# Performance work log

Hardware: AMD Instinct MI355X
Metric: run time of the kernel (lower is better)

Reference implementation:

```python
import jax, jax.numpy as jnp
import numpy as np

TEMP1, TEMP2, TEMP3 = 4.0, 5.0, 10.0  # forward() default temps
EPS = 1e-8


def setup_inputs() -> dict:
    key = jax.random.key(0)
    k1, k2 = jax.random.split(key)
    B, L, D = 64, 64, 512
    return {
        "ecg_embs": jax.random.normal(k1, (B, L, D), dtype=jnp.float32),
        "sent_embs": jax.random.normal(k2, (B, L, D), dtype=jnp.float32),
    }


def reference(ecg_embs, sent_embs):
    # Fully-batched version of the original per-sample Python loop.
    # i indexes the sentence (query) sample, j the ecg (context) sample.
    B, L, D = ecg_embs.shape
    # scores[i,j,s,q] = <ecg[j,s,:], sent[i,q,:]>  == contextT @ query in torch
    scores = jnp.einsum('jsd,iqd->ijsq', ecg_embs, sent_embs)
    # 1st softmax over query axis q
    attn = jax.nn.softmax(scores, axis=-1)
    # transpose to (i,j,q,s), temperature-scale, 2nd softmax over source axis s
    attn = jax.nn.softmax(TEMP1 * jnp.swapaxes(attn, -1, -2), axis=-1)  # (i,j,q,s)
    # weightedContext[i,j,q,:] = sum_s attn[i,j,q,s] * ecg[j,s,:]
    wctx = jnp.einsum('ijqs,jsd->ijqd', attn, ecg_embs)
    sent = sent_embs[:, None]  # (i,1,q,d) broadcast over j
    w12 = jnp.sum(sent * wctx, axis=-1)
    w1 = jnp.linalg.norm(sent, axis=-1)
    w2 = jnp.linalg.norm(wctx, axis=-1)
    cos = w12 / jnp.maximum(w1 * w2, EPS)  # (i,j,q)
    # row_sim.mul_(temp2).exp_().sum(dim=1).log() ; similarities[j,i] (cat along dim=1)
    sim = TEMP3 * jnp.log(jnp.sum(jnp.exp(TEMP2 * cos), axis=-1)).T  # (j,i)
    labels = jnp.arange(B)
    logp0 = jax.nn.log_softmax(sim, axis=-1)
    logp1 = jax.nn.log_softmax(sim.T, axis=-1)
    loss0 = -jnp.mean(logp0[labels, labels])
    loss1 = -jnp.mean(logp1[labels, labels])
    # att_maps: list of attn[i] from iteration i == diagonal (i==j) attention,
    # each shaped (1, queryL, ih=1, iw=sourceL); stacked -> (B, 1, L, 1, L)
    att_maps = attn[labels, labels][:, None, :, None, :]
    return (loss0 + loss1) / 2.0, att_maps
```

## Files before the change

kernel.cpp:

```cpp
#include <hip/hip_runtime.h>
#include <math.h>

typedef __attribute__((ext_vector_type(8))) short short8;
typedef __attribute__((ext_vector_type(4))) float f32x4;
typedef unsigned int uint;
typedef unsigned short ushort;

#define T1 4.0f
#define T2 5.0f
#define T3 10.0f
#define EPSF 1e-8f
#define SST 68

__device__ inline ushort f2bf(float x) {
    union { float f; uint u; } a; a.f = x;
    uint r = a.u + 0x7FFFu + ((a.u >> 16) & 1u);
    return (ushort)(r >> 16);
}
__device__ inline float bf2f(ushort h) {
    union { uint u; float f; } a; a.u = ((uint)h) << 16;
    return a.f;
}

#define GLDS(gsrc, ldst) \
    __builtin_amdgcn_global_load_lds( \
        (const __attribute__((address_space(1))) uint*)(gsrc), \
        (__attribute__((address_space(3))) uint*)(ldst), 16, 0, 0)

__global__ __launch_bounds__(256) void prep_kernel(
        const float* __restrict__ ecg, const float* __restrict__ sent,
        char* __restrict__ EH, char* __restrict__ EL,
        char* __restrict__ SH, char* __restrict__ SL, float* __restrict__ w1) {
    __shared__ float partial[256];
    const int bid = blockIdx.x;
    const int tensor = bid >> 6, idx = bid & 63;
    const float* src = (tensor ? sent : ecg) + (size_t)idx * 32768;
    char* dh = (tensor ? SH : EH) + (size_t)idx * 65536;
    char* dl = (tensor ? SL : EL) + (size_t)idx * 65536;
    const int tid = threadIdx.x;
    const int r = tid & 63;
    float s2 = 0.f;
    #pragma unroll
    for (int it = 0; it < 4; it++) {
        int kc = it * 4 + (tid >> 6);
        const float* p = src + r * 512 + kc * 32;
        char* oh = dh + kc * 4096 + r * 64;
        char* ol = dl + kc * 4096 + r * 64;
        #pragma unroll
        for (int c = 0; c < 4; c++) {
            float4 v0 = *(const float4*)(p + c * 8);
            float4 v1 = *(const float4*)(p + c * 8 + 4);
            float x[8] = {v0.x, v0.y, v0.z, v0.w, v1.x, v1.y, v1.z, v1.w};
            uint hw[4], lw[4];
            #pragma unroll
            for (int e = 0; e < 4; e++) {
                float a0 = x[2 * e], a1 = x[2 * e + 1];
                ushort h0 = f2bf(a0), h1 = f2bf(a1);
                hw[e] = (uint)h0 | ((uint)h1 << 16);
                ushort l0 = f2bf(a0 - bf2f(h0)), l1 = f2bf(a1 - bf2f(h1));
                lw[e] = (uint)l0 | ((uint)l1 << 16);
                s2 += a0 * a0 + a1 * a1;
            }
            int phys = (c + (r >> 1)) & 3;
            uint4 H; H.x = hw[0]; H.y = hw[1]; H.z = hw[2]; H.w = hw[3];
            *(uint4*)(oh + phys * 16) = H;
            uint4 L; L.x = lw[0]; L.y = lw[1]; L.z = lw[2]; L.w = lw[3];
            *(uint4*)(ol + phys * 16) = L;
        }
    }
    partial[tid] = s2;
    __syncthreads();
    if (tensor == 1 && tid < 64) {
        float t = partial[tid] + partial[tid + 64] + partial[tid + 128] + partial[tid + 192];
        w1[idx * 64 + tid] = sqrtf(t);
    }
}

__global__ __launch_bounds__(256) void gprep_kernel(
        const char* __restrict__ EH, const char* __restrict__ EL, char* __restrict__ Gp) {
    __shared__ __align__(16) char lds[8192];
    const int j = blockIdx.x;
    const int tid = threadIdx.x;
    const int wv = tid >> 6, lane = tid & 63;
    const int wq = wv >> 1, wn = wv & 1;
    const int quad = lane >> 4, ln = lane & 15;
    const char* srcH = EH + (size_t)j * 65536 + wv * 1024 + lane * 16;
    const char* srcL = EL + (size_t)j * 65536 + wv * 1024 + lane * 16;

    int ao[2], bo[2];
    #pragma unroll
    for (int mi = 0; mi < 2; mi++) {
        int R = 32 * wq + 16 * mi + ln;
        ao[mi] = R * 64 + ((quad + (R >> 1)) & 3) * 16;
    }
    #pragma unroll
    for (int ni = 0; ni < 2; ni++) {
        int R = 32 * wn + 16 * ni + ln;
        bo[ni] = R * 64 + ((quad + (R >> 1)) & 3) * 16;
    }

    f32x4 acc[2][2];
    #pragma unroll
    for (int a = 0; a < 2; a++)
        #pragma unroll
        for (int b = 0; b < 2; b++) acc[a][b] = (f32x4){0.f, 0.f, 0.f, 0.f};

    for (int kc = 0; kc < 16; kc++) {
        GLDS(srcH + (size_t)kc * 4096, lds + wv * 1024);
        GLDS(srcL + (size_t)kc * 4096, lds + 4096 + wv * 1024);
        __syncthreads();
        short8 ah[2], al[2], bh[2], bl[2];
        #pragma unroll
        for (int mi = 0; mi < 2; mi++) {
            ah[mi] = *(const short8*)(lds + ao[mi]);
            al[mi] = *(const short8*)(lds + 4096 + ao[mi]);
        }
        #pragma unroll
        for (int ni = 0; ni < 2; ni++) {
            bh[ni] = *(const short8*)(lds + bo[ni]);
            bl[ni] = *(const short8*)(lds + 4096 + bo[ni]);
        }
        #pragma unroll
        for (int mi = 0; mi < 2; mi++)
            #pragma unroll
            for (int ni = 0; ni < 2; ni++) {
                acc[mi][ni] = __builtin_amdgcn_mfma_f32_16x16x32_bf16(ah[mi], bh[ni], acc[mi][ni], 0, 0, 0);
                acc[mi][ni] = __builtin_amdgcn_mfma_f32_16x16x32_bf16(ah[mi], bl[ni], acc[mi][ni], 0, 0, 0);
                acc[mi][ni] = __builtin_amdgcn_mfma_f32_16x16x32_bf16(al[mi], bh[ni], acc[mi][ni], 0, 0, 0);
            }
        __syncthreads();
    }
    #pragma unroll
    for (int mi = 0; mi < 2; mi++)
        #pragma unroll
        for (int ni = 0; ni < 2; ni++)
            #pragma unroll
            for (int r = 0; r < 4; r++) {
                int t = 32 * wq + 16 * mi + quad * 4 + r;
                int u = 32 * wn + 16 * ni + ln;
                float g = acc[mi][ni][r];
                ushort h = f2bf(g);
                ushort l = f2bf(g - bf2f(h));
                char* base = Gp + (size_t)j * 16384 + t * 128 + (((u >> 3) + t) & 7) * 16 + (u & 7) * 2;
                *(ushort*)base = h;
                *(ushort*)(base + 8192) = l;
            }
}

__global__ __launch_bounds__(256, 4) void pair_kernel(
        const char* __restrict__ EH, const char* __restrict__ EL,
        const char* __restrict__ SH, const char* __restrict__ SL,
        const char* __restrict__ Gp, const float* __restrict__ w1g,
        float* __restrict__ simval, float* __restrict__ out) {

    __shared__ __align__(16) char lds[33792];
    __shared__ __align__(16) float mz[64];
    __shared__ float w12all[256], w2all[256];

    const int tid = threadIdx.x;
    const int bn = blockIdx.x;
    const int xcd = bn & 7, slot = bn >> 3;
    const int T = xcd * 8 + (slot >> 4);
    const int wp = slot & 15;
    const int bi = (T >> 3) * 4 + (wp >> 2);
    const int bj = (T & 7) * 4 + (wp & 3);
    const int i0 = bi * 2, j0 = bj * 2;

    const int wv = tid >> 6, lane = tid & 63;
    const int wq = wv >> 1, wn = wv & 1;
    const int quad = lane >> 4, ln = lane & 15;

    int aoff[4], boff[4];
    #pragma unroll
    for (int mi = 0; mi < 4; mi++) {
        int R = 64 * (mi >> 1) + 32 * wq + 16 * (mi & 1) + ln;
        aoff[mi] = R * 64 + ((quad + (R >> 1)) & 3) * 16;
    }
    #pragma unroll
    for (int ni = 0; ni < 4; ni++) {
        int R = 64 * (ni >> 1) + 32 * wn + 16 * (ni & 1) + ln;
        boff[ni] = 16384 + R * 64 + ((quad + (R >> 1)) & 3) * 16;
    }

    const char* gA; const char* gB; int ldoff;
    if (wv == 0)      { gA = EH + (size_t)j0 * 65536;       gB = EH + (size_t)(j0 + 1) * 65536; ldoff = 0; }
    else if (wv == 1) { gA = EL + (size_t)j0 * 65536;       gB = EL + (size_t)(j0 + 1) * 65536; ldoff = 8192; }
    else if (wv == 2) { gA = SH + (size_t)i0 * 65536;       gB = SH + (size_t)(i0 + 1) * 65536; ldoff = 16384; }
    else              { gA = SL + (size_t)i0 * 65536;       gB = SL + (size_t)(i0 + 1) * 65536; ldoff = 24576; }
    gA += lane * 16; gB += lane * 16;

    f32x4 acc[4][4];
    #pragma unroll
    for (int a = 0; a < 4; a++)
        #pragma unroll
        for (int b = 0; b < 4; b++) acc[a][b] = (f32x4){0.f, 0.f, 0.f, 0.f};

    for (int kc = 0; kc < 16; kc++) {
        #pragma unroll
        for (int n = 0; n < 4; n++) GLDS(gA + n * 1024, lds + ldoff + n * 1024);
        #pragma unroll
        for (int n = 0; n < 4; n++) GLDS(gB + n * 1024, lds + ldoff + 4096 + n * 1024);
        gA += 4096; gB += 4096;
        __syncthreads();
        short8 bh[4], bl[4];
        #pragma unroll
        for (int ni = 0; ni < 4; ni++) {
            bh[ni] = *(const short8*)(lds + boff[ni]);
            bl[ni] = *(const short8*)(lds + boff[ni] + 8192);
        }
        #pragma unroll
        for (int mi = 0; mi < 4; mi++) {
            short8 ah = *(const short8*)(lds + aoff[mi]);
            short8 al = *(const short8*)(lds + aoff[mi] + 8192);
            #pragma unroll
            for (int ni = 0; ni < 4; ni++) {
                acc[mi][ni] = __builtin_amdgcn_mfma_f32_16x16x32_bf16(ah, bh[ni], acc[mi][ni], 0, 0, 0);
                acc[mi][ni] = __builtin_amdgcn_mfma_f32_16x16x32_bf16(ah, bl[ni], acc[mi][ni], 0, 0, 0);
                acc[mi][ni] = __builtin_amdgcn_mfma_f32_16x16x32_bf16(al, bh[ni], acc[mi][ni], 0, 0, 0);
            }
        }
        __syncthreads();
    }

    float* SsT = (float*)lds;
    float* yT  = (float*)lds;
    char*  Pb  = lds + 17408;

    #pragma unroll
    for (int pr = 0; pr < 4; pr++) {
        const int a = pr >> 1, b = pr & 1;
        const int i = i0 + b, j = j0 + a;

        #pragma unroll
        for (int dm = 0; dm < 2; dm++)
            #pragma unroll
            for (int dn = 0; dn < 2; dn++) {
                int s0 = 32 * wq + 16 * dm + quad * 4;
                int q  = 32 * wn + 16 * dn + ln;
                *(f32x4*)(SsT + q * SST + s0) = acc[2 * a + dm][2 * b + dn];
            }
        __syncthreads();

        {
            const int s = tid >> 2, c = tid & 3;
            float vv[16]; float m = -1e30f;
            #pragma unroll
            for (int t = 0; t < 16; t++) { vv[t] = SsT[(16 * c + t) * SST + s]; m = fmaxf(m, vv[t]); }
            m = fmaxf(m, __shfl_xor(m, 1));
            m = fmaxf(m, __shfl_xor(m, 2));
            float sum = 0.f;
            #pragma unroll
            for (int t = 0; t < 16; t++) sum += __expf(vv[t] - m);
            sum += __shfl_xor(sum, 1);
            sum += __shfl_xor(sum, 2);
            if (c == 0) mz[s] = m + __logf(sum);
        }
        __syncthreads();

        {
            const int q = tid >> 2, c = tid & 3;
            float sc[16], at[16];
            #pragma unroll
            for (int r4 = 0; r4 < 4; r4++)
                *(f32x4*)(sc + 4 * r4) = *(const f32x4*)(SsT + q * SST + 16 * c + 4 * r4);
            float mzv[16];
            #pragma unroll
            for (int r4 = 0; r4 < 4; r4++)
                *(f32x4*)(mzv + 4 * r4) = *(const f32x4*)(mz + 16 * c + 4 * r4);
            float m2 = -1e30f;
            #pragma unroll
            for (int t = 0; t < 16; t++) {
                at[t] = __expf(sc[t] - mzv[t]);
                m2 = fmaxf(m2, T1 * at[t]);
            }
            m2 = fmaxf(m2, __shfl_xor(m2, 1));
            m2 = fmaxf(m2, __shfl_xor(m2, 2));
            float sum = 0.f;
            #pragma unroll
            for (int t = 0; t < 16; t++) { at[t] = __expf(T1 * at[t] - m2); sum += at[t]; }
            sum += __shfl_xor(sum, 1);
            sum += __shfl_xor(sum, 2);
            float inv = 1.f / sum;
            float p12 = 0.f;
            #pragma unroll
            for (int t = 0; t < 16; t++) { at[t] *= inv; p12 += at[t] * sc[t]; }
            p12 += __shfl_xor(p12, 1);
            p12 += __shfl_xor(p12, 2);
            if (c == 0) w12all[pr * 64 + q] = p12;

            if (i == j) {
                float* om = out + 1 + (size_t)i * 4096;
                #pragma unroll
                for (int t = 0; t < 16; t++) om[q * 64 + c * 16 + t] = at[t];
            }

            uint hw[8], lw[8];
            #pragma unroll
            for (int e = 0; e < 8; e++) {
                ushort h0 = f2bf(at[2 * e]), h1 = f2bf(at[2 * e + 1]);
                hw[e] = (uint)h0 | ((uint)h1 << 16);
                ushort l0 = f2bf(at[2 * e] - bf2f(h0)), l1 = f2bf(at[2 * e + 1] - bf2f(h1));
                lw[e] = (uint)l0 | ((uint)l1 << 16);
            }
            int p0 = (2 * c + q) & 7, p1 = (2 * c + 1 + q) & 7;
            uint4 W;
            W.x = hw[0]; W.y = hw[1]; W.z = hw[2]; W.w = hw[3];
            *(uint4*)(Pb + q * 128 + p0 * 16) = W;
            W.x = hw[4]; W.y = hw[5]; W.z = hw[6]; W.w = hw[7];
            *(uint4*)(Pb + q * 128 + p1 * 16) = W;
            W.x = lw[0]; W.y = lw[1]; W.z = lw[2]; W.w = lw[3];
            *(uint4*)(Pb + 8192 + q * 128 + p0 * 16) = W;
            W.x = lw[4]; W.y = lw[5]; W.z = lw[6]; W.w = lw[7];
            *(uint4*)(Pb + 8192 + q * 128 + p1 * 16) = W;
        }
        __syncthreads();

        {
            const char* gs = Gp + (size_t)j * 16384 + tid * 64;
            char* gd = lds + tid * 64;
            uint4 g0 = *(const uint4*)(gs);
            uint4 g1 = *(const uint4*)(gs + 16);
            uint4 g2 = *(const uint4*)(gs + 32);
            uint4 g3 = *(const uint4*)(gs + 48);
            *(uint4*)(gd)      = g0;
            *(uint4*)(gd + 16) = g1;
            *(uint4*)(gd + 32) = g2;
            *(uint4*)(gd + 48) = g3;
        }
        __syncthreads();

        f32x4 acc2[2][2];
        #pragma unroll
        for (int x = 0; x < 2; x++)
            #pragma unroll
            for (int y = 0; y < 2; y++) acc2[x][y] = (f32x4){0.f, 0.f, 0.f, 0.f};
        #pragma unroll
        for (int ch = 0; ch < 2; ch++) {
            short8 pah[2], pal[2], gbh[2], gbl[2];
            #pragma unroll
            for (int m2i = 0; m2i < 2; m2i++) {
                int q = 32 * wq + 16 * m2i + ln;
                int ph = ((ch * 4 + quad) + q) & 7;
                pah[m2i] = *(const short8*)(Pb + q * 128 + ph * 16);
                pal[m2i] = *(const short8*)(Pb + 8192 + q * 128 + ph * 16);
            }
            #pragma unroll
            for (int n2i = 0; n2i < 2; n2i++) {
                int u = 32 * wn + 16 * n2i + ln;
                int ph = ((ch * 4 + quad) + u) & 7;
                gbh[n2i] = *(const short8*)(lds + u * 128 + ph * 16);
                gbl[n2i] = *(const short8*)(lds + 8192 + u * 128 + ph * 16);
            }
            #pragma unroll
            for (int m2i = 0; m2i < 2; m2i++)
                #pragma unroll
                for (int n2i = 0; n2i < 2; n2i++) {
                    acc2[m2i][n2i] = __builtin_amdgcn_mfma_f32_16x16x32_bf16(pah[m2i], gbh[n2i], acc2[m2i][n2i], 0, 0, 0);
                    acc2[m2i][n2i] = __builtin_amdgcn_mfma_f32_16x16x32_bf16(pah[m2i], gbl[n2i], acc2[m2i][n2i], 0, 0, 0);
                    acc2[m2i][n2i] = __builtin_amdgcn_mfma_f32_16x16x32_bf16(pal[m2i], gbh[n2i], acc2[m2i][n2i], 0, 0, 0);
                }
        }
        __syncthreads();

        #pragma unroll
        for (int m2i = 0; m2i < 2; m2i++)
            #pragma unroll
            for (int n2i = 0; n2i < 2; n2i++) {
                int q0 = 32 * wq + 16 * m2i + quad * 4;
                int t  = 32 * wn + 16 * n2i + ln;
                *(f32x4*)(yT + t * SST + q0) = acc2[m2i][n2i];
            }
        __syncthreads();

        {
            const int q = tid >> 2, c = tid & 3;
            int p0 = (2 * c + q) & 7, p1 = (2 * c + 1 + q) & 7;
            uint4 H0 = *(const uint4*)(Pb + q * 128 + p0 * 16);
            uint4 H1 = *(const uint4*)(Pb + q * 128 + p1 * 16);
            uint4 L0 = *(const uint4*)(Pb + 8192 + q * 128 + p0 * 16);
            uint4 L1 = *(const uint4*)(Pb + 8192 + q * 128 + p1 * 16);
            uint hw[8] = {H0.x,H0.y,H0.z,H0.w, H1.x,H1.y,H1.z,H1.w};
            uint lw[8] = {L0.x,L0.y,L0.z,L0.w, L1.x,L1.y,L1.z,L1.w};
            float s = 0.f;
            #pragma unroll
            for (int e = 0; e < 8; e++) {
                float q0v = bf2f((ushort)(hw[e] & 0xFFFFu)) + bf2f((ushort)(lw[e] & 0xFFFFu));
                float q1v = bf2f((ushort)(hw[e] >> 16))     + bf2f((ushort)(lw[e] >> 16));
                s += q0v * yT[(16 * c + 2 * e) * SST + q];
                s += q1v * yT[(16 * c + 2 * e + 1) * SST + q];
            }
            s += __shfl_xor(s, 1);
            s += __shfl_xor(s, 2);
            if (c == 0) w2all[pr * 64 + q] = s;
        }
        __syncthreads();
    }

    {
        const int pr = wv;
        const int ii = i0 + (pr & 1), jj = j0 + (pr >> 1);
        float w2 = sqrtf(fmaxf(w2all[pr * 64 + lane], 0.f));
        float cosv = w12all[pr * 64 + lane] / fmaxf(w1g[ii * 64 + lane] * w2, EPSF);
        float e = __expf(T2 * cosv);
        #pragma unroll
        for (int off = 32; off; off >>= 1) e += __shfl_down(e, off);
        if (lane == 0) simval[ii * 64 + jj] = T3 * __logf(e);
    }
}

__global__ __launch_bounds__(256) void loss_kernel(const float* __restrict__ val,
                                                   float* __restrict__ out) {
    __shared__ float v[4096];
    const int tid = threadIdx.x;
    #pragma unroll
    for (int k = 0; k < 4; k++)
        ((float4*)v)[tid + k * 256] = ((const float4*)val)[tid + k * 256];
    __syncthreads();
    if (tid < 64) {
        int i = tid;
        float rmax = -1e30f, cmax = -1e30f;
        for (int jj = 0; jj < 64; jj++) {
            rmax = fmaxf(rmax, v[i * 64 + jj]);
            cmax = fmaxf(cmax, v[jj * 64 + i]);
        }
        float rs = 0.f, cs = 0.f;
        for (int jj = 0; jj < 64; jj++) {
            rs += __expf(v[i * 64 + jj] - rmax);
            cs += __expf(v[jj * 64 + i] - cmax);
        }
        float rlse = rmax + __logf(rs);
        float clse = cmax + __logf(cs);
        float part = 2.f * v[i * 64 + i] - rlse - clse;
        #pragma unroll
        for (int off = 32; off; off >>= 1) part += __shfl_down(part, off);
        if (i == 0) out[0] = -part / 128.f;
    }
}

extern "C" void kernel_launch(void* const* d_in, const int* in_sizes, int n_in,
                              void* d_out, int out_size, void* d_ws, size_t ws_size,
                              hipStream_t stream) {
    (void)in_sizes; (void)n_in; (void)out_size; (void)ws_size;
    const float* ecg  = (const float*)d_in[0];
    const float* sent = (const float*)d_in[1];
    float* out = (float*)d_out;

    char* ws = (char*)d_ws;
    float* w1v  = (float*)ws;
    float* simv = (float*)(ws + 16384);
    char* EH = ws + 32768;
    char* EL = EH + (size_t)64 * 65536;
    char* SH = EL + (size_t)64 * 65536;
    char* SL = SH + (size_t)64 * 65536;
    char* Gp = SL + (size_t)64 * 65536;

    prep_kernel <<<128, 256, 0, stream>>>(ecg, sent, EH, EL, SH, SL, w1v);
    gprep_kernel<<<64,  256, 0, stream>>>(EH, EL, Gp);
    pair_kernel <<<1024, 256, 0, stream>>>(EH, EL, SH, SL, Gp, w1v, simv, out);
    loss_kernel <<<1,   256, 0, stream>>>(simv, out);
}
```

Before: 152.3 us.

## Fuse Gram prep into prep kernel and loss into pair kernel via atomic counter

Folds the ecg Gram-matrix computation into prep_kernel (ecg blocks read back their just-written bf16 data from global instead of staging through LDS). The loss reduction moves into the last-finishing pair_kernel block, detected with an atomic counter, which drops two launches. Inside pair_kernel the Gp copy now uses global_load_lds, the y tile is stored q-major so the w2 dot product can use vector LDS reads, and the softmax column reads are rotated per lane to reduce bank conflicts. In exchange it relies on threadfence ordering for the last-block reduction and on intra-block global read-after-write visibility in prep.

```diff
diff --git a/kernel.cpp b/kernel.cpp
--- a/kernel.cpp
+++ b/kernel.cpp
@@ -30,10 +30,12 @@
 __global__ __launch_bounds__(256) void prep_kernel(
         const float* __restrict__ ecg, const float* __restrict__ sent,
         char* __restrict__ EH, char* __restrict__ EL,
-        char* __restrict__ SH, char* __restrict__ SL, float* __restrict__ w1) {
+        char* __restrict__ SH, char* __restrict__ SL,
+        char* __restrict__ Gp, float* __restrict__ w1, uint* __restrict__ donecnt) {
     __shared__ float partial[256];
     const int bid = blockIdx.x;
     const int tensor = bid >> 6, idx = bid & 63;
+    if (bid == 0 && threadIdx.x == 0) *donecnt = 0;
     const float* src = (tensor ? sent : ecg) + (size_t)idx * 32768;
     char* dh = (tensor ? SH : EH) + (size_t)idx * 65536;
     char* dl = (tensor ? SL : EL) + (size_t)idx * 65536;
@@ -70,92 +72,91 @@
     }
     partial[tid] = s2;
     __syncthreads();
-    if (tensor == 1 && tid < 64) {
-        float t = partial[tid] + partial[tid + 64] + partial[tid + 128] + partial[tid + 192];
-        w1[idx * 64 + tid] = sqrtf(t);
-    }
-}
-
-__global__ __launch_bounds__(256) void gprep_kernel(
-        const char* __restrict__ EH, const char* __restrict__ EL, char* __restrict__ Gp) {
-    __shared__ __align__(16) char lds[8192];
-    const int j = blockIdx.x;
-    const int tid = threadIdx.x;
-    const int wv = tid >> 6, lane = tid & 63;
-    const int wq = wv >> 1, wn = wv & 1;
-    const int quad = lane >> 4, ln = lane & 15;
-    const char* srcH = EH + (size_t)j * 65536 + wv * 1024 + lane * 16;
-    const char* srcL = EL + (size_t)j * 65536 + wv * 1024 + lane * 16;
-
-    int ao[2], bo[2];
-    #pragma unroll
-    for (int mi = 0; mi < 2; mi++) {
-        int R = 32 * wq + 16 * mi + ln;
-        ao[mi] = R * 64 + ((quad + (R >> 1)) & 3) * 16;
-    }
-    #pragma unroll
-    for (int ni = 0; ni < 2; ni++) {
-        int R = 32 * wn + 16 * ni + ln;
-        bo[ni] = R * 64 + ((quad + (R >> 1)) & 3) * 16;
-    }
-
-    f32x4 acc[2][2];
-    #pragma unroll
-    for (int a = 0; a < 2; a++)
-        #pragma unroll
-        for (int b = 0; b < 2; b++) acc[a][b] = (f32x4){0.f, 0.f, 0.f, 0.f};
-
-    for (int kc = 0; kc < 16; kc++) {
-        GLDS(srcH + (size_t)kc * 4096, lds + wv * 1024);
-        GLDS(srcL + (size_t)kc * 4096, lds + 4096 + wv * 1024);
-        __syncthreads();
-        short8 ah[2], al[2], bh[2], bl[2];
+    if (tensor == 1) {
+        if (tid < 64) {
+            float t = partial[tid] + partial[tid + 64] + partial[tid + 128] + partial[tid + 192];
+            w1[idx * 64 + tid] = sqrtf(t);
+        }
+        return;
+    }
+
+    {
+        const char* srcH = EH + (size_t)idx * 65536;
+        const char* srcL = EL + (size_t)idx * 65536;
+        const int wv = tid >> 6, lane = tid & 63;
+        const int wq = wv >> 1, wn = wv & 1;
+        const int quad = lane >> 4, ln = lane & 15;
+
+        int ao[2], bo[2];
         #pragma unroll
         for (int mi = 0; mi < 2; mi++) {
-            ah[mi] = *(const short8*)(lds + ao[mi]);
-            al[mi] = *(const short8*)(lds + 4096 + ao[mi]);
+            int R = 32 * wq + 16 * mi + ln;
+            ao[mi] = R * 64 + ((quad + (R >> 1)) & 3) * 16;
         }
         #pragma unroll
         for (int ni = 0; ni < 2; ni++) {
-            bh[ni] = *(const short8*)(lds + bo[ni]);
-            bl[ni] = *(const short8*)(lds + 4096 + bo[ni]);
+            int R = 32 * wn + 16 * ni + ln;
+            bo[ni] = R * 64 + ((quad + (R >> 1)) & 3) * 16;
+        }
+
+        f32x4 acc[2][2];
+        #pragma unroll
+        for (int a = 0; a < 2; a++)
+            #pragma unroll
+            for (int b = 0; b < 2; b++) acc[a][b] = (f32x4){0.f, 0.f, 0.f, 0.f};
+
+        #pragma unroll 2
+        for (int kc = 0; kc < 16; kc++) {
+            const char* ph = srcH + (size_t)kc * 4096;
+            const char* pl = srcL + (size_t)kc * 4096;
+            short8 ah[2], al[2], bh[2], bl[2];
+            #pragma unroll
+            for (int mi = 0; mi < 2; mi++) {
+                ah[mi] = *(const short8*)(ph + ao[mi]);
+                al[mi] = *(const short8*)(pl + ao[mi]);
+            }
+            #pragma unroll
+            for (int ni = 0; ni < 2; ni++) {
+                bh[ni] = *(const short8*)(ph + bo[ni]);
+                bl[ni] = *(const short8*)(pl + bo[ni]);
+            }
+            #pragma unroll
+            for (int mi = 0; mi < 2; mi++)
+                #pragma unroll
+                for (int ni = 0; ni < 2; ni++) {
+                    acc[mi][ni] = __builtin_amdgcn_mfma_f32_16x16x32_bf16(ah[mi], bh[ni], acc[mi][ni], 0, 0, 0);
+                    acc[mi][ni] = __builtin_amdgcn_mfma_f32_16x16x32_bf16(ah[mi], bl[ni], acc[mi][ni], 0, 0, 0);
+                    acc[mi][ni] = __builtin_amdgcn_mfma_f32_16x16x32_bf16(al[mi], bh[ni], acc[mi][ni], 0, 0, 0);
+                }
         }
         #pragma unroll
         for (int mi = 0; mi < 2; mi++)
             #pragma unroll
-            for (int ni = 0; ni < 2; ni++) {
-                acc[mi][ni] = __builtin_amdgcn_mfma_f32_16x16x32_bf16(ah[mi], bh[ni], acc[mi][ni], 0, 0, 0);
-                acc[mi][ni] = __builtin_amdgcn_mfma_f32_16x16x32_bf16(ah[mi], bl[ni], acc[mi][ni], 0, 0, 0);
-                acc[mi][ni] = __builtin_amdgcn_mfma_f32_16x16x32_bf16(al[mi], bh[ni], acc[mi][ni], 0, 0, 0);
-            }
-        __syncthreads();
-    }
-    #pragma unroll
-    for (int mi = 0; mi < 2; mi++)
-        #pragma unroll
-        for (int ni = 0; ni < 2; ni++)
-            #pragma unroll
-            for (int r = 0; r < 4; r++) {
-                int t = 32 * wq + 16 * mi + quad * 4 + r;
-                int u = 32 * wn + 16 * ni + ln;
-                float g = acc[mi][ni][r];
-                ushort h = f2bf(g);
-                ushort l = f2bf(g - bf2f(h));
-                char* base = Gp + (size_t)j * 16384 + t * 128 + (((u >> 3) + t) & 7) * 16 + (u & 7) * 2;
-                *(ushort*)base = h;
-                *(ushort*)(base + 8192) = l;
-            }
+            for (int ni = 0; ni < 2; ni++)
+                #pragma unroll
+                for (int rr = 0; rr < 4; rr++) {
+                    int t = 32 * wq + 16 * mi + quad * 4 + rr;
+                    int u = 32 * wn + 16 * ni + ln;
+                    float g = acc[mi][ni][rr];
+                    ushort h = f2bf(g);
+                    ushort l = f2bf(g - bf2f(h));
+                    char* base = Gp + (size_t)idx * 16384 + t * 128 + (((u >> 3) + t) & 7) * 16 + (u & 7) * 2;
+                    *(ushort*)base = h;
+                    *(ushort*)(base + 8192) = l;
+                }
+    }
 }
 
 __global__ __launch_bounds__(256, 4) void pair_kernel(
         const char* __restrict__ EH, const char* __restrict__ EL,
         const char* __restrict__ SH, const char* __restrict__ SL,
         const char* __restrict__ Gp, const float* __restrict__ w1g,
-        float* __restrict__ simval, float* __restrict__ out) {
+        float* __restrict__ simval, float* __restrict__ out, uint* __restrict__ donecnt) {
 
     __shared__ __align__(16) char lds[33792];
     __shared__ __align__(16) float mz[64];
     __shared__ float w12all[256], w2all[256];
+    __shared__ uint lastflag;
 
     const int tid = threadIdx.x;
     const int bn = blockIdx.x;
@@ -223,7 +224,7 @@
     }
 
     float* SsT = (float*)lds;
-    float* yT  = (float*)lds;
+    float* yQ  = (float*)lds;
     char*  Pb  = lds + 17408;
 
     #pragma unroll
@@ -245,7 +246,11 @@
             const int s = tid >> 2, c = tid & 3;
             float vv[16]; float m = -1e30f;
             #pragma unroll
-            for (int t = 0; t < 16; t++) { vv[t] = SsT[(16 * c + t) * SST + s]; m = fmaxf(m, vv[t]); }
+            for (int t = 0; t < 16; t++) {
+                int tt = (t + 4 * c) & 15;
+                vv[t] = SsT[(16 * c + tt) * SST + s];
+                m = fmaxf(m, vv[t]);
+            }
             m = fmaxf(m, __shfl_xor(m, 1));
             m = fmaxf(m, __shfl_xor(m, 2));
             float sum = 0.f;
@@ -316,16 +321,12 @@
         __syncthreads();
 
         {
-            const char* gs = Gp + (size_t)j * 16384 + tid * 64;
-            char* gd = lds + tid * 64;
-            uint4 g0 = *(const uint4*)(gs);
-            uint4 g1 = *(const uint4*)(gs + 16);
-            uint4 g2 = *(const uint4*)(gs + 32);
-            uint4 g3 = *(const uint4*)(gs + 48);
-            *(uint4*)(gd)      = g0;
-            *(uint4*)(gd + 16) = g1;
-            *(uint4*)(gd + 32) = g2;
-            *(uint4*)(gd + 48) = g3;
+            const char* gs = Gp + (size_t)j * 16384 + wv * 4096 + lane * 16;
+            char* gd = lds + wv * 4096;
+            GLDS(gs,        gd);
+            GLDS(gs + 1024, gd + 1024);
+            GLDS(gs + 2048, gd + 2048);
+            GLDS(gs + 3072, gd + 3072);
         }
         __syncthreads();
 
@@ -366,9 +367,12 @@
         for (int m2i = 0; m2i < 2; m2i++)
             #pragma unroll
             for (int n2i = 0; n2i < 2; n2i++) {
-                int q0 = 32 * wq + 16 * m2i + quad * 4;
                 int t  = 32 * wn + 16 * n2i + ln;
-                *(f32x4*)(yT + t * SST + q0) = acc2[m2i][n2i];
+                int qb = 32 * wq + 16 * m2i + quad * 4;
+                yQ[(qb + 0) * SST + t] = acc2[m2i][n2i][0];
+                yQ[(qb + 1) * SST + t] = acc2[m2i][n2i][1];
+                yQ[(qb + 2) * SST + t] = acc2[m2i][n2i][2];
+                yQ[(qb + 3) * SST + t] = acc2[m2i][n2i][3];
             }
         __syncthreads();
 
@@ -381,13 +385,17 @@
             uint4 L1 = *(const uint4*)(Pb + 8192 + q * 128 + p1 * 16);
             uint hw[8] = {H0.x,H0.y,H0.z,H0.w, H1.x,H1.y,H1.z,H1.w};
             uint lw[8] = {L0.x,L0.y,L0.z,L0.w, L1.x,L1.y,L1.z,L1.w};
+            float vy[16];
+            #pragma unroll
+            for (int r4 = 0; r4 < 4; r4++)
+                *(f32x4*)(vy + 4 * r4) = *(const f32x4*)(yQ + q * SST + 16 * c + 4 * r4);
             float s = 0.f;
             #pragma unroll
             for (int e = 0; e < 8; e++) {
                 float q0v = bf2f((ushort)(hw[e] & 0xFFFFu)) + bf2f((ushort)(lw[e] & 0xFFFFu));
                 float q1v = bf2f((ushort)(hw[e] >> 16))     + bf2f((ushort)(lw[e] >> 16));
-                s += q0v * yT[(16 * c + 2 * e) * SST + q];
-                s += q1v * yT[(16 * c + 2 * e + 1) * SST + q];
+                s += q0v * vy[2 * e];
+                s += q1v * vy[2 * e + 1];
             }
             s += __shfl_xor(s, 1);
             s += __shfl_xor(s, 2);
@@ -406,34 +414,40 @@
         for (int off = 32; off; off >>= 1) e += __shfl_down(e, off);
         if (lane == 0) simval[ii * 64 + jj] = T3 * __logf(e);
     }
-}
-
-__global__ __launch_bounds__(256) void loss_kernel(const float* __restrict__ val,
-                                                   float* __restrict__ out) {
-    __shared__ float v[4096];
-    const int tid = threadIdx.x;
-    #pragma unroll
-    for (int k = 0; k < 4; k++)
-        ((float4*)v)[tid + k * 256] = ((const float4*)val)[tid + k * 256];
     __syncthreads();
-    if (tid < 64) {
-        int i = tid;
-        float rmax = -1e30f, cmax = -1e30f;
-        for (int jj = 0; jj < 64; jj++) {
-            rmax = fmaxf(rmax, v[i * 64 + jj]);
-            cmax = fmaxf(cmax, v[jj * 64 + i]);
-        }
-        float rs = 0.f, cs = 0.f;
-        for (int jj = 0; jj < 64; jj++) {
-            rs += __expf(v[i * 64 + jj] - rmax);
-            cs += __expf(v[jj * 64 + i] - cmax);
-        }
-        float rlse = rmax + __logf(rs);
-        float clse = cmax + __logf(cs);
-        float part = 2.f * v[i * 64 + i] - rlse - clse;
-        #pragma unroll
-        for (int off = 32; off; off >>= 1) part += __shfl_down(part, off);
-        if (i == 0) out[0] = -part / 128.f;
+
+    if (tid == 0) {
+        __threadfence();
+        uint prev = atomicAdd(donecnt, 1u);
+        lastflag = (prev == 1023u);
+    }
+    __syncthreads();
+    if (lastflag) {
+        __threadfence();
+        float* v = (float*)lds;
+        #pragma unroll
+        for (int k = 0; k < 4; k++)
+            ((float4*)v)[tid + k * 256] = ((const float4*)simval)[tid + k * 256];
+        __syncthreads();
+        if (tid < 64) {
+            int i = tid;
+            float rmax = -1e30f, cmax = -1e30f;
+            for (int jj = 0; jj < 64; jj++) {
+                rmax = fmaxf(rmax, v[i * 64 + jj]);
+                cmax = fmaxf(cmax, v[jj * 64 + i]);
+            }
+            float rs = 0.f, cs = 0.f;
+            for (int jj = 0; jj < 64; jj++) {
+                rs += __expf(v[i * 64 + jj] - rmax);
+                cs += __expf(v[jj * 64 + i] - cmax);
+            }
+            float rlse = rmax + __logf(rs);
+            float clse = cmax + __logf(cs);
+            float part = 2.f * v[i * 64 + i] - rlse - clse;
+            #pragma unroll
+            for (int off = 32; off; off >>= 1) part += __shfl_down(part, off);
+            if (i == 0) out[0] = -part / 128.f;
+        }
     }
 }
 
@@ -448,14 +462,13 @@
     char* ws = (char*)d_ws;
     float* w1v  = (float*)ws;
     float* simv = (float*)(ws + 16384);
-    char* EH = ws + 32768;
+    uint*  dcnt = (uint*)(ws + 32768);
+    char* EH = ws + 33024;
     char* EL = EH + (size_t)64 * 65536;
     char* SH = EL + (size_t)64 * 65536;
     char* SL = SH + (size_t)64 * 65536;
     char* Gp = SL + (size_t)64 * 65536;
 
-    prep_kernel <<<128, 256, 0, stream>>>(ecg, sent, EH, EL, SH, SL, w1v);
-    gprep_kernel<<<64,  256, 0, stream>>>(EH, EL, Gp);
-    pair_kernel <<<1024, 256, 0, stream>>>(EH, EL, SH, SL, Gp, w1v, simv, out);
-    loss_kernel <<<1,   256, 0, stream>>>(simv, out);
+    prep_kernel <<<128, 256, 0, stream>>>(ecg, sent, EH, EL, SH, SL, Gp, w1v, dcnt);
+    pair_kernel <<<1024, 256, 0, stream>>>(EH, EL, SH, SL, Gp, w1v, simv, out, dcnt);
 }
```

Result: slower. 165.2 us (+8.4%).
